# Optimization experiments

Hardware: AMD Instinct MI355X
Metric: run time of the kernel (lower is better)

The kernel has to match this reference:

```python
import jax, jax.numpy as jnp
import numpy as np

N = 50000      # nodes
E = 600000     # edges (avg degree 12)
D_IN = 16      # node_input_size
D = 128        # hidden_size
H = 4          # num_heads
DH = D // H
L = 4          # message_passing_num
D_FF = 512     # 4*hidden FFN expansion
D_OUT = 3      # output_size


def setup_inputs() -> dict:
    key = jax.random.key(0)
    ks = iter(jax.random.split(key, 32))
    def w(shape, fan_in):
        return jax.random.normal(next(ks), shape, jnp.float32) / np.float32(np.sqrt(fan_in))
    return {
        "features": jax.random.normal(next(ks), (N, D_IN), jnp.float32),
        "senders": jax.random.randint(next(ks), (E,), 0, N),
        "receivers": jax.random.randint(next(ks), (E,), 0, N),
        "enc_w1": w((D_IN, D), D_IN), "enc_b1": jnp.zeros((D,), jnp.float32),
        "enc_w2": w((D, D), D),       "enc_b2": jnp.zeros((D,), jnp.float32),
        "wq": w((L, D, D), D), "wk": w((L, D, D), D),
        "wv": w((L, D, D), D), "wo": w((L, D, D), D),
        "ln1_s": jnp.ones((L, D), jnp.float32), "ln1_b": jnp.zeros((L, D), jnp.float32),
        "ffn_w1": w((L, D, D_FF), D), "ffn_b1": jnp.zeros((L, D_FF), jnp.float32),
        "ffn_w2": w((L, D_FF, D), D_FF), "ffn_b2": jnp.zeros((L, D), jnp.float32),
        "ln2_s": jnp.ones((L, D), jnp.float32), "ln2_b": jnp.zeros((L, D), jnp.float32),
        "dec_w1": w((D, D_OUT), D), "dec_b1": jnp.zeros((D_OUT,), jnp.float32),
        "dec_w2": w((D_OUT, D_OUT), D_OUT), "dec_b2": jnp.zeros((D_OUT,), jnp.float32),
    }


def _ln(x, s, b):
    mu = x.mean(-1, keepdims=True)
    var = ((x - mu) ** 2).mean(-1, keepdims=True)
    return (x - mu) * jax.lax.rsqrt(var + 1e-5) * s + b


def _graph_mha(x, senders, receivers, wq, wk, wv, wo):
    # Adjacency-masked attention done sparsely over the edge list
    # (equivalent to softmax over the BCOO adjacency pattern).
    n = x.shape[0]
    q = (x @ wq).reshape(n, H, DH)
    k = (x @ wk).reshape(n, H, DH)
    v = (x @ wv).reshape(n, H, DH)
    scores = (q[receivers] * k[senders]).sum(-1) / np.float32(np.sqrt(DH))  # [E,H]
    m = jax.ops.segment_max(scores, receivers, num_segments=n)             # [N,H]
    m = jnp.where(jnp.isfinite(m), m, 0.0)
    a = jnp.exp(scores - m[receivers])                                      # [E,H]
    denom = jax.ops.segment_sum(a, receivers, num_segments=n)              # [N,H]
    msg = jax.ops.segment_sum(a[:, :, None] * v[senders], receivers, num_segments=n)  # [N,H,DH]
    out = (msg / (denom[:, :, None] + 1e-9)).reshape(n, D)
    return out @ wo


def reference(features, senders, receivers,
              enc_w1, enc_b1, enc_w2, enc_b2,
              wq, wk, wv, wo, ln1_s, ln1_b,
              ffn_w1, ffn_b1, ffn_w2, ffn_b2, ln2_s, ln2_b,
              dec_w1, dec_b1, dec_w2, dec_b2):
    # encode
    x = jnp.maximum(features @ enc_w1 + enc_b1, 0.0) @ enc_w2 + enc_b2     # [N,D]
    # process: L pre-LN sparse-attention transformer blocks
    for l in range(L):
        h = _ln(x, ln1_s[l], ln1_b[l])
        x = x + _graph_mha(h, senders, receivers, wq[l], wk[l], wv[l], wo[l])
        h = _ln(x, ln2_s[l], ln2_b[l])
        x = x + jnp.maximum(h @ ffn_w1[l] + ffn_b1[l], 0.0) @ ffn_w2[l] + ffn_b2[l]
    # decode
    return jnp.maximum(x @ dec_w1 + dec_b1, 0.0) @ dec_w2 + dec_b2         # [N,D_OUT]
```

## Files before the change

### kernel.cpp

```cpp
#include <hip/hip_runtime.h>
#include <hip/hip_bf16.h>
#include <math.h>

#define D     128
#define NHEAD 4
#define DH    32
#define DFF   512
#define DIN   16
#define MAXDEG 64
#define TN    16

typedef __attribute__((ext_vector_type(8))) short bf16x8;
typedef __attribute__((ext_vector_type(4))) float f32x4;
typedef __hip_bfloat16 bf16;

#define QSCALE_L2E 0.2550348838f

#define BM 128

#define WAITV(N) asm volatile("s_waitcnt vmcnt(" #N ")" ::: "memory")
#define WAITLGKM asm volatile("s_waitcnt lgkmcnt(0)" ::: "memory")
#define FENCE()  asm volatile("" ::: "memory")
#define BAR() do { FENCE(); __builtin_amdgcn_s_barrier(); FENCE(); } while (0)

__device__ __forceinline__ void gll16(const bf16* g, bf16* l) {
    __builtin_amdgcn_global_load_lds((__attribute__((address_space(1))) void*)g,
                                     (__attribute__((address_space(3))) void*)l,
                                     16, 0, 0);
}

__device__ __forceinline__ ushort bfbits(float f) {
    __hip_bfloat16 b = __float2bfloat16(f);
    return *(ushort*)&b;
}

__global__ void k_fill(const int* __restrict__ recv, const int* __restrict__ senders,
                       int* __restrict__ deg, int* __restrict__ eid, int E) {
    int e = blockIdx.x * blockDim.x + threadIdx.x;
    if (e >= E) return;
    int r = recv[e];
    int pos = atomicAdd(&deg[r], 1);
    if (pos < MAXDEG) eid[r * MAXDEG + pos] = senders[e];
}

__global__ void k_wt(const float* __restrict__ wq, const float* __restrict__ wk,
                     const float* __restrict__ wv, const float* __restrict__ wo,
                     const float* __restrict__ w1, const float* __restrict__ w2,
                     const float* __restrict__ encw2,
                     bf16* __restrict__ wqkvT, bf16* __restrict__ woT,
                     bf16* __restrict__ w1T, bf16* __restrict__ w2T,
                     bf16* __restrict__ encw2T, int* __restrict__ deg, int N) {
    int r = blockIdx.y;
    if (r == 25) {
        int i = blockIdx.x * blockDim.x + threadIdx.x;
        if (i < N) deg[i] = 0;
        return;
    }
    const float* src; bf16* dst; int K, Nout;
    if (r < 12) {
        int l = r / 3, sel = r % 3;
        src = (sel == 0 ? wq : sel == 1 ? wk : wv) + (size_t)l * D * D;
        dst = wqkvT + (size_t)l * 3 * D * D + (size_t)sel * D * D;
        K = D; Nout = D;
    } else if (r < 16) {
        int l = r - 12;
        src = wo + (size_t)l * D * D; dst = woT + (size_t)l * D * D; K = D; Nout = D;
    } else if (r < 20) {
        int l = r - 16;
        src = w1 + (size_t)l * D * DFF; dst = w1T + (size_t)l * D * DFF; K = D; Nout = DFF;
    } else if (r < 24) {
        int l = r - 20;
        src = w2 + (size_t)l * DFF * D; dst = w2T + (size_t)l * DFF * D; K = DFF; Nout = D;
    } else {
        src = encw2; dst = encw2T; K = D; Nout = D;
    }
    int total = K * Nout;
    int i = blockIdx.x * blockDim.x + threadIdx.x;
    if (i >= total) return;
    int k = i / Nout, j = i % Nout;
    dst[(size_t)j * K + k] = __float2bfloat16(src[i]);
}

__device__ __forceinline__ void load_afrag(const bf16* A, int arow, int quad,
                                           int N, bf16x8* afr) {
    const bf16* ab = A + (size_t)arow * D + quad * 8;
#pragma unroll
    for (int i = 0; i < 4; i++) {
        uint4 v = make_uint4(0u, 0u, 0u, 0u);
        if (arow < N) v = *(const uint4*)(ab + i * 32);
        afr[i] = *(bf16x8*)&v;
    }
}

__device__ __forceinline__ void stage_full(bf16* lb, const bf16* src,
                                           int wave, int lane) {
#pragma unroll
    for (int k = 0; k < 4; k++) {
        int gidx = (wave * 4 + k) * 64 + lane;
        int r = gidx >> 4, gL = gidx & 15;
        gll16(src + (size_t)r * 128 + ((gL ^ (r & 15)) * 8),
              lb + (size_t)(wave * 4 + k) * 512);
    }
}

__device__ __forceinline__ void stage_half(bf16* lb, const bf16* src, int rs,
                                           int wave, int lane) {
#pragma unroll
    for (int k = 0; k < 2; k++) {
        int gidx = (wave * 2 + k) * 64 + lane;
        int r = gidx >> 3, gL = gidx & 7;
        gll16(src + (size_t)r * rs + ((gL ^ (r & 7)) * 8),
              lb + (size_t)(wave * 2 + k) * 512);
    }
}

__device__ __forceinline__ void mfma_tile(const bf16* Wb, const bf16x8* afr,
                                          f32x4* acc, int l16, int quad) {
#pragma unroll
    for (int i = 0; i < 4; i++)
#pragma unroll
        for (int j = 0; j < 8; j++) {
            const bf16* wp = Wb + (size_t)(j * 16 + l16) * 128
                              + (size_t)((((i * 4 + quad)) ^ l16) * 8);
            acc[j] = __builtin_amdgcn_mfma_f32_16x16x32_bf16(afr[i], *(const bf16x8*)wp,
                                                             acc[j], 0, 0, 0);
        }
}

template<int OP>
__global__ __launch_bounds__(512, 2) void k_gemm(
        const bf16* __restrict__ A, const bf16* __restrict__ Bt,
        const float* __restrict__ bias,
        const float* __restrict__ lns, const float* __restrict__ lnb,
        float* x, bf16* outB, int N) {
    __shared__ alignas(16) bf16 Wsm[128 * 128];
    int m0 = blockIdx.x * BM;
    int t = threadIdx.x;
    int wave = t >> 6, lane = t & 63;
    int quad = lane >> 4, l16 = lane & 15;
    int wm = wave * 16;

    bf16x8 afr[4];
    load_afrag(A, m0 + wm + l16, quad, N, afr);
    FENCE();
    stage_full(Wsm, Bt, wave, lane);
    WAITV(0); BAR();

    int rowb = m0 + wm + quad * 4;
    float xv[8][4];
    if (OP == 2) {
#pragma unroll
        for (int j = 0; j < 8; j++)
#pragma unroll
            for (int r = 0; r < 4; r++) {
                int gr = rowb + r;
                xv[j][r] = (gr < N) ? x[(size_t)gr * D + j * 16 + l16] : 0.f;
            }
    }

    f32x4 acc[8];
#pragma unroll
    for (int j = 0; j < 8; j++) acc[j] = (f32x4){0.f, 0.f, 0.f, 0.f};
    mfma_tile(Wsm, afr, acc, l16, quad);

    float bv[8];
    if (OP == 5) {
#pragma unroll
        for (int j = 0; j < 8; j++) bv[j] = bias[j * 16 + l16];
    }
#pragma unroll
    for (int j = 0; j < 8; j++) {
#pragma unroll
        for (int r = 0; r < 4; r++) {
            int gr = rowb + r;
            if (gr >= N) continue;
            float val = acc[j][r];
            if (OP == 5) val += bv[j];
            if (OP == 2) val += xv[j][r];
            acc[j][r] = val;
        }
    }
    float lsv[8], lbv[8];
#pragma unroll
    for (int j = 0; j < 8; j++) {
        lsv[j] = lns[j * 16 + l16];
        lbv[j] = lnb[j * 16 + l16];
    }
#pragma unroll
    for (int r = 0; r < 4; r++) {
        float s1 = 0.f, s2 = 0.f;
#pragma unroll
        for (int j = 0; j < 8; j++) {
            float v = acc[j][r];
            s1 += v; s2 += v * v;
        }
        s1 += __shfl_xor(s1, 1, 64);  s2 += __shfl_xor(s2, 1, 64);
        s1 += __shfl_xor(s1, 2, 64);  s2 += __shfl_xor(s2, 2, 64);
        s1 += __shfl_xor(s1, 4, 64);  s2 += __shfl_xor(s2, 4, 64);
        s1 += __shfl_xor(s1, 8, 64);  s2 += __shfl_xor(s2, 8, 64);
        float mu = s1 * (1.f / 128.f);
        float var = s2 * (1.f / 128.f) - mu * mu;
        float rinv = rsqrtf(fmaxf(var, 0.f) + 1e-5f);
        int gr = rowb + r;
        if (gr >= N) continue;
#pragma unroll
        for (int j = 0; j < 8; j++) {
            int col = j * 16 + l16;
            float v = acc[j][r];
            x[(size_t)gr * D + col] = v;
            outB[(size_t)gr * D + col] =
                __float2bfloat16((v - mu) * rinv * lsv[j] + lbv[j]);
        }
    }
}

__global__ __launch_bounds__(512, 2) void k_qkv(
        const bf16* __restrict__ hb, const bf16* __restrict__ wqkvT,
        bf16* __restrict__ qb, bf16* __restrict__ kvb, int N) {
    __shared__ alignas(16) bf16 Wbuf[2][128 * 128];
    int m0 = blockIdx.x * BM;
    int t = threadIdx.x;
    int wave = t >> 6, lane = t & 63;
    int quad = lane >> 4, l16 = lane & 15;
    int wm = wave * 16;

    bf16x8 afr[4];
    load_afrag(hb, m0 + wm + l16, quad, N, afr);
    FENCE();
    stage_full(Wbuf[0], wqkvT + (size_t)D * D, wave, lane);
    FENCE();
    stage_full(Wbuf[1], wqkvT + (size_t)2 * D * D, wave, lane);
    FENCE();

    int rowb = m0 + wm + quad * 4;
    f32x4 ak[8], acc[8];
#pragma unroll
    for (int j = 0; j < 8; j++) ak[j] = (f32x4){0.f, 0.f, 0.f, 0.f};

    WAITV(4); BAR();
    __builtin_amdgcn_s_setprio(1);
    mfma_tile(Wbuf[0], afr, ak, l16, quad);
    __builtin_amdgcn_s_setprio(0);
    BAR();
    stage_full(Wbuf[0], wqkvT, wave, lane);
    FENCE();
#pragma unroll
    for (int j = 0; j < 8; j++) acc[j] = (f32x4){0.f, 0.f, 0.f, 0.f};
    WAITV(4); BAR();
    __builtin_amdgcn_s_setprio(1);
    mfma_tile(Wbuf[1], afr, acc, l16, quad);
    __builtin_amdgcn_s_setprio(0);

#pragma unroll
    for (int j = 0; j < 8; j++) {
        int col = j * 16 + l16;
#pragma unroll
        for (int r = 0; r < 4; r++) {
            int gr = rowb + r;
            if (gr >= N) continue;
            uint kv = (uint)bfbits(ak[j][r]) | ((uint)bfbits(acc[j][r]) << 16);
            *(uint*)&kvb[((size_t)gr * D + col) * 2] = kv;
        }
    }
    FENCE();
    if (m0 + BM <= N) { WAITV(32); } else { WAITV(0); }
    BAR();
#pragma unroll
    for (int j = 0; j < 8; j++) acc[j] = (f32x4){0.f, 0.f, 0.f, 0.f};
    __builtin_amdgcn_s_setprio(1);
    mfma_tile(Wbuf[0], afr, acc, l16, quad);
    __builtin_amdgcn_s_setprio(0);
#pragma unroll
    for (int j = 0; j < 8; j++) {
        int col = j * 16 + l16;
#pragma unroll
        for (int r = 0; r < 4; r++) {
            int gr = rowb + r;
            if (gr >= N) continue;
            qb[(size_t)gr * D + col] = __float2bfloat16(acc[j][r] * QSCALE_L2E);
        }
    }
}

__device__ __forceinline__ void stage_ffn_tile(int ts, const bf16* w1T,
                                               const bf16* w2T, bf16* Wb3,
                                               int wave, int lane) {
    int c = ts >> 2, ph = ts & 3;
    const bf16* src; int rs;
    if (ph < 2) { src = w1T + (size_t)(c * 128) * 128 + ph * 64; rs = 128; }
    else        { src = w2T + c * 128 + (ph - 2) * 64;           rs = DFF; }
    stage_half(Wb3 + (size_t)(ts % 3) * (64 * 128), src, rs, wave, lane);
}

template<int MODE>
__global__ __launch_bounds__(512, 2) void k_ffn(
        const bf16* __restrict__ hb, const bf16* __restrict__ w1T,
        const float* __restrict__ b1,
        const bf16* __restrict__ w2T, const float* __restrict__ b2,
        const float* __restrict__ lns, const float* __restrict__ lnb,
        const float* __restrict__ dw1, const float* __restrict__ db1,
        const float* __restrict__ dw2, const float* __restrict__ db2,
        float* x, bf16* outB, float* out, int N) {
    __shared__ alignas(16) bf16 Wb3[3][64 * 128];
    __shared__ alignas(16) bf16 Hsm[128 * 128];
    int m0 = blockIdx.x * BM;
    int t = threadIdx.x;
    int wave = t >> 6, lane = t & 63;
    int quad = lane >> 4, l16 = lane & 15;
    int wm = wave * 16;
    int rowb = m0 + wm + quad * 4;

    float b1pre[4][8];
#pragma unroll
    for (int c2 = 0; c2 < 4; c2++)
#pragma unroll
        for (int j = 0; j < 8; j++) b1pre[c2][j] = b1[c2 * 128 + j * 16 + l16];

    bf16x8 afr[4];
    load_afrag(hb, m0 + wm + l16, quad, N, afr);
    FENCE();
    stage_ffn_tile(0, w1T, w2T, &Wb3[0][0], wave, lane);
    FENCE();
    stage_ffn_tile(1, w1T, w2T, &Wb3[0][0], wave, lane);
    FENCE();

    f32x4 acc2[8], accP[8];
#pragma unroll
    for (int j = 0; j < 8; j++) acc2[j] = (f32x4){0.f, 0.f, 0.f, 0.f};
    float xv[8][4];

#pragma unroll
    for (int s = 0; s < 16; s++) {
        BAR();
        if (s + 2 < 16) {
            stage_ffn_tile(s + 2, w1T, w2T, &Wb3[0][0], wave, lane);
            FENCE();
        }
        if (s < 14) { WAITV(4); } else if (s == 14) { WAITV(2); } else { WAITV(0); }
        BAR();
        const bf16* Wb = &Wb3[0][0] + (size_t)(s % 3) * (64 * 128);
        int c = s >> 2, ph = s & 3;
        if (s == 15) {
#pragma unroll
            for (int j = 0; j < 8; j++)
#pragma unroll
                for (int r = 0; r < 4; r++) {
                    int gr = rowb + r;
                    xv[j][r] = (gr < N) ? x[(size_t)gr * D + j * 16 + l16] : 0.f;
                }
        }
        if (ph < 2) {
            if (ph == 0) {
#pragma unroll
                for (int j = 0; j < 8; j++) accP[j] = (f32x4){0.f, 0.f, 0.f, 0.f};
            }
            __builtin_amdgcn_s_setprio(1);
#pragma unroll
            for (int i2 = 0; i2 < 2; i2++) {
#pragma unroll
                for (int j = 0; j < 8; j++) {
                    const bf16* wp = Wb + (size_t)(j * 16 + l16) * 64
                                      + (size_t)(((i2 * 4 + quad) ^ (l16 & 7)) * 8);
                    accP[j] = __builtin_amdgcn_mfma_f32_16x16x32_bf16(
                        afr[ph * 2 + i2], *(const bf16x8*)wp, accP[j], 0, 0, 0);
                }
            }
            __builtin_amdgcn_s_setprio(0);
            if (ph == 1) {
                int rw = wm + quad * 4;
#pragma unroll
                for (int j = 0; j < 8; j++) {
                    int gb = j * 2 + (l16 >> 3), ce = l16 & 7;
#pragma unroll
                    for (int r = 0; r < 4; r++) {
                        int row = rw + r;
                        Hsm[(size_t)row * 128 + (size_t)((gb ^ (row & 15)) * 8) + ce] =
                            __float2bfloat16(fmaxf(accP[j][r] + b1pre[c][j], 0.f));
                    }
                }
                WAITLGKM;
            }
        } else {
            int h = ph - 2;
            __builtin_amdgcn_s_setprio(1);
#pragma unroll
            for (int k2 = 0; k2 < 2; k2++) {
                int ks = h * 2 + k2;
                const bf16* hp = Hsm + (size_t)(wm + l16) * 128
                                  + (size_t)(((ks * 4 + quad) ^ l16) * 8);
                bf16x8 af2 = *(const bf16x8*)hp;
#pragma unroll
                for (int j = 0; j < 8; j++) {
                    const bf16* wp = Wb + (size_t)(j * 16 + l16) * 64
                                      + (size_t)(((k2 * 4 + quad) ^ (l16 & 7)) * 8);
                    acc2[j] = __builtin_amdgcn_mfma_f32_16x16x32_bf16(
                        af2, *(const bf16x8*)wp, acc2[j], 0, 0, 0);
                }
            }
            __builtin_amdgcn_s_setprio(0);
        }
    }

    float bv[8];
#pragma unroll
    for (int j = 0; j < 8; j++) bv[j] = b2[j * 16 + l16];
#pragma unroll
    for (int j = 0; j < 8; j++) {
#pragma unroll
        for (int r = 0; r < 4; r++) {
            int gr = rowb + r;
            if (gr >= N) continue;
            acc2[j][r] += bv[j] + xv[j][r];
        }
    }
    if (MODE == 1) {
        float dw[8][3];
#pragma unroll
        for (int j = 0; j < 8; j++) {
            int col = j * 16 + l16;
#pragma unroll
            for (int cc3 = 0; cc3 < 3; cc3++) dw[j][cc3] = dw1[col * 3 + cc3];
        }
#pragma unroll
        for (int r = 0; r < 4; r++) {
            float s0 = 0.f, s1 = 0.f, s2 = 0.f;
#pragma unroll
            for (int j = 0; j < 8; j++) {
                float v = acc2[j][r];
                s0 += v * dw[j][0]; s1 += v * dw[j][1]; s2 += v * dw[j][2];
            }
            s0 += __shfl_xor(s0, 1, 64); s1 += __shfl_xor(s1, 1, 64); s2 += __shfl_xor(s2, 1, 64);
            s0 += __shfl_xor(s0, 2, 64); s1 += __shfl_xor(s1, 2, 64); s2 += __shfl_xor(s2, 2, 64);
            s0 += __shfl_xor(s0, 4, 64); s1 += __shfl_xor(s1, 4, 64); s2 += __shfl_xor(s2, 4, 64);
            s0 += __shfl_xor(s0, 8, 64); s1 += __shfl_xor(s1, 8, 64); s2 += __shfl_xor(s2, 8, 64);
            int gr = rowb + r;
            if (l16 == 0 && gr < N) {
                float t0 = fmaxf(s0 + db1[0], 0.f);
                float t1 = fmaxf(s1 + db1[1], 0.f);
                float t2 = fmaxf(s2 + db1[2], 0.f);
#pragma unroll
                for (int o = 0; o < 3; o++)
                    out[(size_t)gr * 3 + o] =
                        t0 * dw2[0 * 3 + o] + t1 * dw2[1 * 3 + o] + t2 * dw2[2 * 3 + o] + db2[o];
            }
        }
        return;
    }
    float lsv[8], lbv[8];
#pragma unroll
    for (int j = 0; j < 8; j++) {
        lsv[j] = lns[j * 16 + l16];
        lbv[j] = lnb[j * 16 + l16];
    }
#pragma unroll
    for (int r = 0; r < 4; r++) {
        float s1 = 0.f, s2 = 0.f;
#pragma unroll
        for (int j = 0; j < 8; j++) {
            float v = acc2[j][r];
            s1 += v; s2 += v * v;
        }
        s1 += __shfl_xor(s1, 1, 64);  s2 += __shfl_xor(s2, 1, 64);
        s1 += __shfl_xor(s1, 2, 64);  s2 += __shfl_xor(s2, 2, 64);
        s1 += __shfl_xor(s1, 4, 64);  s2 += __shfl_xor(s2, 4, 64);
        s1 += __shfl_xor(s1, 8, 64);  s2 += __shfl_xor(s2, 8, 64);
        float mu = s1 * (1.f / 128.f);
        float var = s2 * (1.f / 128.f) - mu * mu;
        float rinv = rsqrtf(fmaxf(var, 0.f) + 1e-5f);
        int gr = rowb + r;
        if (gr >= N) continue;
#pragma unroll
        for (int j = 0; j < 8; j++) {
            int col = j * 16 + l16;
            float v = acc2[j][r];
            x[(size_t)gr * D + col] = v;
            outB[(size_t)gr * D + col] = __float2bfloat16((v - mu) * rinv * lsv[j] + lbv[j]);
        }
    }
}

__global__ void k_enc1(const float* __restrict__ feat,
                       const float* __restrict__ w1, const float* __restrict__ b1,
                       bf16* __restrict__ hb, int N) {
    __shared__ float fsh[TN][DIN];
    int n0 = blockIdx.x * TN;
    int j = threadIdx.x;
    int nvalid = min(TN, N - n0);
    for (int idx = j; idx < TN * DIN; idx += 128) {
        int n = idx / DIN, i = idx % DIN;
        fsh[n][i] = (n < nvalid) ? feat[(n0 + n) * DIN + i] : 0.f;
    }
    __syncthreads();
    float bb = b1[j];
#pragma unroll
    for (int n = 0; n < TN; n++) {
        float a = bb;
#pragma unroll
        for (int i = 0; i < DIN; i++) a += fsh[n][i] * w1[i * D + j];
        if (n < nvalid) hb[(size_t)(n0 + n) * D + j] = __float2bfloat16(fmaxf(a, 0.f));
    }
}

__device__ __forceinline__ void attn_edge(uint4 w, bool v, float4 qv,
                                          float& l, float& a0, float& a1,
                                          float& a2, float& a3) {
    float k0 = __uint_as_float(w.x << 16), v0 = __uint_as_float(w.x & 0xFFFF0000u);
    float k1 = __uint_as_float(w.y << 16), v1 = __uint_as_float(w.y & 0xFFFF0000u);
    float k2 = __uint_as_float(w.z << 16), v2 = __uint_as_float(w.z & 0xFFFF0000u);
    float k3 = __uint_as_float(w.w << 16), v3 = __uint_as_float(w.w & 0xFFFF0000u);
    float p = qv.x * k0 + qv.y * k1 + qv.z * k2 + qv.w * k3;
    p += __shfl_xor(p, 1, 64);
    p += __shfl_xor(p, 2, 64);
    p += __shfl_xor(p, 4, 64);
    float e = v ? exp2f(p) : 0.f;
    l += e;
    a0 += e * v0; a1 += e * v1; a2 += e * v2; a3 += e * v3;
}

__global__ __launch_bounds__(256) void k_attn(
        const bf16* __restrict__ qb, const uint* __restrict__ kvb,
        const int* __restrict__ deg, const int* __restrict__ eid,
        bf16* __restrict__ out, int N) {
    int wave = threadIdx.x >> 6, lane = threadIdx.x & 63;
    int r = blockIdx.x * 4 + wave;
    if (r >= N) return;
    int g = lane & 7;
    int h = (lane >> 3) & 3;
    int slot = lane >> 5;
    int d0 = h * 32 + g * 4;
    uint2 qw = *(const uint2*)(qb + (size_t)r * D + d0);
    float4 qv;
    qv.x = __uint_as_float(qw.x << 16);
    qv.y = __uint_as_float(qw.x & 0xFFFF0000u);
    qv.z = __uint_as_float(qw.y << 16);
    qv.w = __uint_as_float(qw.y & 0xFFFF0000u);
    int cnt = min(deg[r], MAXDEG);
    const int* row = eid + (size_t)r * MAXDEG;
    const uint* kvbase = kvb + d0;
    float l = 0.f, a0 = 0.f, a1 = 0.f, a2 = 0.f, a3 = 0.f;
    for (int base = 0; base < cnt; base += 16) {
        int ss[8];
        bool vv[8];
#pragma unroll
        for (int u = 0; u < 8; u++) {
            int e = base + u * 2 + slot;
            vv[u] = e < cnt;
            ss[u] = vv[u] ? row[e] : 0;
        }
        uint4 w[8];
#pragma unroll
        for (int u = 0; u < 8; u++)
            w[u] = *(const uint4*)(kvbase + (size_t)ss[u] * D);
#pragma unroll
        for (int u = 0; u < 8; u++)
            attn_edge(w[u], vv[u], qv, l, a0, a1, a2, a3);
    }
    l  += __shfl_xor(l, 32, 64);
    a0 += __shfl_xor(a0, 32, 64);
    a1 += __shfl_xor(a1, 32, 64);
    a2 += __shfl_xor(a2, 32, 64);
    a3 += __shfl_xor(a3, 32, 64);
    if (lane < 32) {
        float inv = 1.f / (l + 1e-9f);
        bf16 o[4];
        o[0] = __float2bfloat16(a0 * inv);
        o[1] = __float2bfloat16(a1 * inv);
        o[2] = __float2bfloat16(a2 * inv);
        o[3] = __float2bfloat16(a3 * inv);
        *(uint2*)(out + (size_t)r * D + d0) = *(uint2*)o;
    }
}

extern "C" void kernel_launch(void* const* d_in, const int* in_sizes, int n_in,
                              void* d_out, int out_size, void* d_ws, size_t ws_size,
                              hipStream_t stream) {
    const float* feat    = (const float*)d_in[0];
    const int*   senders = (const int*)d_in[1];
    const int*   recv    = (const int*)d_in[2];
    const float* enc_w1  = (const float*)d_in[3];
    const float* enc_b1  = (const float*)d_in[4];
    const float* enc_w2  = (const float*)d_in[5];
    const float* enc_b2  = (const float*)d_in[6];
    const float* wq      = (const float*)d_in[7];
    const float* wk      = (const float*)d_in[8];
    const float* wv      = (const float*)d_in[9];
    const float* wo      = (const float*)d_in[10];
    const float* ln1_s   = (const float*)d_in[11];
    const float* ln1_b   = (const float*)d_in[12];
    const float* ffn_w1  = (const float*)d_in[13];
    const float* ffn_b1  = (const float*)d_in[14];
    const float* ffn_w2  = (const float*)d_in[15];
    const float* ffn_b2  = (const float*)d_in[16];
    const float* ln2_s   = (const float*)d_in[17];
    const float* ln2_b   = (const float*)d_in[18];
    const float* dec_w1  = (const float*)d_in[19];
    const float* dec_b1  = (const float*)d_in[20];
    const float* dec_w2  = (const float*)d_in[21];
    const float* dec_b2  = (const float*)d_in[22];

    int N = in_sizes[0] / DIN;
    int E = in_sizes[1];

    char* p = (char*)d_ws;
    float* x   = (float*)p;  p += (size_t)N * D * 4;
    bf16*  qb  = (bf16*)p;   p += (size_t)N * D * 2;
    bf16*  kvb = (bf16*)p;   p += (size_t)N * D * 2 * 2;
    bf16*  hb  = (bf16*)p;   p += (size_t)N * D * 2;
    int* deg   = (int*)p;    p += (size_t)N * 4;
    int* eid   = (int*)p;    p += (size_t)N * MAXDEG * 4;
    bf16* wqkvT  = (bf16*)p; p += (size_t)4 * 3 * D * D * 2;
    bf16* woT    = (bf16*)p; p += (size_t)4 * D * D * 2;
    bf16* w1T    = (bf16*)p; p += (size_t)4 * D * DFF * 2;
    bf16* w2T    = (bf16*)p; p += (size_t)4 * DFF * D * 2;
    bf16* encw2T = (bf16*)p; p += (size_t)D * D * 2;

    int gm = (N + BM - 1) / BM;

    k_wt<<<dim3(256, 26), 256, 0, stream>>>(wq, wk, wv, wo, ffn_w1, ffn_w2, enc_w2,
                                            wqkvT, woT, w1T, w2T, encw2T, deg, N);
    k_fill<<<(E + 255) / 256, 256, 0, stream>>>(recv, senders, deg, eid, E);
    k_enc1<<<(N + TN - 1) / TN, 128, 0, stream>>>(feat, enc_w1, enc_b1, hb, N);
    k_gemm<5><<<gm, 512, 0, stream>>>(hb, encw2T, enc_b2, ln1_s, ln1_b, x, hb, N);

    for (int l = 0; l < 4; l++) {
        k_qkv<<<gm, 512, 0, stream>>>(hb, wqkvT + (size_t)l * 3 * D * D, qb, kvb, N);
        k_attn<<<(N + 3) / 4, 256, 0, stream>>>(qb, (const uint*)kvb, deg, eid, hb, N);
        k_gemm<2><<<gm, 512, 0, stream>>>(hb, woT + (size_t)l * D * D,
                                          nullptr, ln2_s + l * D, ln2_b + l * D,
                                          x, hb, N);
        if (l < 3)
            k_ffn<0><<<gm, 512, 0, stream>>>(hb, w1T + (size_t)l * D * DFF,
                                             ffn_b1 + l * DFF,
                                             w2T + (size_t)l * DFF * D, ffn_b2 + l * D,
                                             ln1_s + (l + 1) * D, ln1_b + (l + 1) * D,
                                             nullptr, nullptr, nullptr, nullptr,
                                             x, hb, nullptr, N);
        else
            k_ffn<1><<<gm, 512, 0, stream>>>(hb, w1T + (size_t)l * D * DFF,
                                             ffn_b1 + l * DFF,
                                             w2T + (size_t)l * DFF * D, ffn_b2 + l * D,
                                             nullptr, nullptr,
                                             dec_w1, dec_b1, dec_w2, dec_b2,
                                             x, nullptr, (float*)d_out, N);
    }
}
```

Measured before the change: 611.6 us.

## Shrink GEMM/FFN tiles to 64 rows with 256 threads; batch attention rows with prefetch

```diff
diff --git a/kernel.cpp b/kernel.cpp
--- a/kernel.cpp
+++ b/kernel.cpp
@@ -16,7 +16,7 @@
 
 #define QSCALE_L2E 0.2550348838f
 
-#define BM 128
+#define BMQ 128
 
 #define WAITV(N) asm volatile("s_waitcnt vmcnt(" #N ")" ::: "memory")
 #define WAITLGKM asm volatile("s_waitcnt lgkmcnt(0)" ::: "memory")
@@ -49,11 +49,16 @@
                      const float* __restrict__ encw2,
                      bf16* __restrict__ wqkvT, bf16* __restrict__ woT,
                      bf16* __restrict__ w1T, bf16* __restrict__ w2T,
-                     bf16* __restrict__ encw2T, int* __restrict__ deg, int N) {
+                     bf16* __restrict__ encw2T, int* __restrict__ deg,
+                     int* __restrict__ eid, int N) {
     int r = blockIdx.y;
     if (r == 25) {
-        int i = blockIdx.x * blockDim.x + threadIdx.x;
-        if (i < N) deg[i] = 0;
+        int tot = N + N * MAXDEG;
+        for (int i = blockIdx.x * blockDim.x + threadIdx.x; i < tot;
+             i += 256 * 256) {
+            if (i < N) deg[i] = 0;
+            else eid[i - N] = 0;
+        }
         return;
     }
     const float* src; bf16* dst; int K, Nout;
@@ -92,8 +97,19 @@
     }
 }
 
-__device__ __forceinline__ void stage_full(bf16* lb, const bf16* src,
-                                           int wave, int lane) {
+__device__ __forceinline__ void stage_full256(bf16* lb, const bf16* src,
+                                              int wave, int lane) {
+#pragma unroll
+    for (int k = 0; k < 8; k++) {
+        int gidx = (wave * 8 + k) * 64 + lane;
+        int r = gidx >> 4, gL = gidx & 15;
+        gll16(src + (size_t)r * 128 + ((gL ^ (r & 15)) * 8),
+              lb + (size_t)(wave * 8 + k) * 512);
+    }
+}
+
+__device__ __forceinline__ void stage_full512(bf16* lb, const bf16* src,
+                                              int wave, int lane) {
 #pragma unroll
     for (int k = 0; k < 4; k++) {
         int gidx = (wave * 4 + k) * 64 + lane;
@@ -103,13 +119,13 @@
     }
 }
 
-__device__ __forceinline__ void stage_half(bf16* lb, const bf16* src, int rs,
-                                           int wave, int lane) {
+__device__ __forceinline__ void stage_q(bf16* lb, const bf16* src, int rs,
+                                        int wave, int lane) {
 #pragma unroll
     for (int k = 0; k < 2; k++) {
         int gidx = (wave * 2 + k) * 64 + lane;
-        int r = gidx >> 3, gL = gidx & 7;
-        gll16(src + (size_t)r * rs + ((gL ^ (r & 7)) * 8),
+        int r = gidx >> 2, gL = gidx & 3;
+        gll16(src + (size_t)r * rs + ((gL ^ ((r >> 1) & 3)) * 8),
               lb + (size_t)(wave * 2 + k) * 512);
     }
 }
@@ -128,13 +144,13 @@
 }
 
 template<int OP>
-__global__ __launch_bounds__(512, 2) void k_gemm(
+__global__ __launch_bounds__(256, 4) void k_gemm(
         const bf16* __restrict__ A, const bf16* __restrict__ Bt,
         const float* __restrict__ bias,
         const float* __restrict__ lns, const float* __restrict__ lnb,
         float* x, bf16* outB, int N) {
     __shared__ alignas(16) bf16 Wsm[128 * 128];
-    int m0 = blockIdx.x * BM;
+    int m0 = blockIdx.x * 64;
     int t = threadIdx.x;
     int wave = t >> 6, lane = t & 63;
     int quad = lane >> 4, l16 = lane & 15;
@@ -143,7 +159,7 @@
     bf16x8 afr[4];
     load_afrag(A, m0 + wm + l16, quad, N, afr);
     FENCE();
-    stage_full(Wsm, Bt, wave, lane);
+    stage_full256(Wsm, Bt, wave, lane);
     WAITV(0); BAR();
 
     int rowb = m0 + wm + quad * 4;
@@ -218,7 +234,7 @@
         const bf16* __restrict__ hb, const bf16* __restrict__ wqkvT,
         bf16* __restrict__ qb, bf16* __restrict__ kvb, int N) {
     __shared__ alignas(16) bf16 Wbuf[2][128 * 128];
-    int m0 = blockIdx.x * BM;
+    int m0 = blockIdx.x * BMQ;
     int t = threadIdx.x;
     int wave = t >> 6, lane = t & 63;
     int quad = lane >> 4, l16 = lane & 15;
@@ -227,9 +243,9 @@
     bf16x8 afr[4];
     load_afrag(hb, m0 + wm + l16, quad, N, afr);
     FENCE();
-    stage_full(Wbuf[0], wqkvT + (size_t)D * D, wave, lane);
-    FENCE();
-    stage_full(Wbuf[1], wqkvT + (size_t)2 * D * D, wave, lane);
+    stage_full512(Wbuf[0], wqkvT + (size_t)D * D, wave, lane);
+    FENCE();
+    stage_full512(Wbuf[1], wqkvT + (size_t)2 * D * D, wave, lane);
     FENCE();
 
     int rowb = m0 + wm + quad * 4;
@@ -242,7 +258,7 @@
     mfma_tile(Wbuf[0], afr, ak, l16, quad);
     __builtin_amdgcn_s_setprio(0);
     BAR();
-    stage_full(Wbuf[0], wqkvT, wave, lane);
+    stage_full512(Wbuf[0], wqkvT, wave, lane);
     FENCE();
 #pragma unroll
     for (int j = 0; j < 8; j++) acc[j] = (f32x4){0.f, 0.f, 0.f, 0.f};
@@ -263,7 +279,7 @@
         }
     }
     FENCE();
-    if (m0 + BM <= N) { WAITV(32); } else { WAITV(0); }
+    if (m0 + BMQ <= N) { WAITV(32); } else { WAITV(0); }
     BAR();
 #pragma unroll
     for (int j = 0; j < 8; j++) acc[j] = (f32x4){0.f, 0.f, 0.f, 0.f};
@@ -282,18 +298,18 @@
     }
 }
 
-__device__ __forceinline__ void stage_ffn_tile(int ts, const bf16* w1T,
-                                               const bf16* w2T, bf16* Wb3,
-                                               int wave, int lane) {
-    int c = ts >> 2, ph = ts & 3;
+__device__ __forceinline__ void stage_ffn_q(int ts, const bf16* w1T,
+                                            const bf16* w2T, bf16* Wb3,
+                                            int wave, int lane) {
+    int c = ts >> 3, p = ts & 7;
     const bf16* src; int rs;
-    if (ph < 2) { src = w1T + (size_t)(c * 128) * 128 + ph * 64; rs = 128; }
-    else        { src = w2T + c * 128 + (ph - 2) * 64;           rs = DFF; }
-    stage_half(Wb3 + (size_t)(ts % 3) * (64 * 128), src, rs, wave, lane);
+    if (p < 4) { src = w1T + (size_t)(c * 128) * 128 + p * 32;       rs = 128; }
+    else       { src = w2T + (size_t)(c * 128) + (p - 4) * 32;       rs = DFF; }
+    stage_q(Wb3 + (size_t)(ts % 3) * (32 * 128), src, rs, wave, lane);
 }
 
 template<int MODE>
-__global__ __launch_bounds__(512, 2) void k_ffn(
+__global__ __launch_bounds__(256, 4) void k_ffn(
         const bf16* __restrict__ hb, const bf16* __restrict__ w1T,
         const float* __restrict__ b1,
         const bf16* __restrict__ w2T, const float* __restrict__ b2,
@@ -301,9 +317,9 @@
         const float* __restrict__ dw1, const float* __restrict__ db1,
         const float* __restrict__ dw2, const float* __restrict__ db2,
         float* x, bf16* outB, float* out, int N) {
-    __shared__ alignas(16) bf16 Wb3[3][64 * 128];
-    __shared__ alignas(16) bf16 Hsm[128 * 128];
-    int m0 = blockIdx.x * BM;
+    __shared__ alignas(16) bf16 Wb3[3][32 * 128];
+    __shared__ alignas(16) bf16 Hsm[64 * 128];
+    int m0 = blockIdx.x * 64;
     int t = threadIdx.x;
     int wave = t >> 6, lane = t & 63;
     int quad = lane >> 4, l16 = lane & 15;
@@ -319,9 +335,9 @@
     bf16x8 afr[4];
     load_afrag(hb, m0 + wm + l16, quad, N, afr);
     FENCE();
-    stage_ffn_tile(0, w1T, w2T, &Wb3[0][0], wave, lane);
-    FENCE();
-    stage_ffn_tile(1, w1T, w2T, &Wb3[0][0], wave, lane);
+    stage_ffn_q(0, w1T, w2T, &Wb3[0][0], wave, lane);
+    FENCE();
+    stage_ffn_q(1, w1T, w2T, &Wb3[0][0], wave, lane);
     FENCE();
 
     f32x4 acc2[8], accP[8];
@@ -329,18 +345,20 @@
     for (int j = 0; j < 8; j++) acc2[j] = (f32x4){0.f, 0.f, 0.f, 0.f};
     float xv[8][4];
 
-#pragma unroll
-    for (int s = 0; s < 16; s++) {
+    int wswz = (quad ^ ((l16 >> 1) & 3)) * 8;
+
+#pragma unroll
+    for (int s = 0; s < 32; s++) {
         BAR();
-        if (s + 2 < 16) {
-            stage_ffn_tile(s + 2, w1T, w2T, &Wb3[0][0], wave, lane);
+        if (s + 2 < 32) {
+            stage_ffn_q(s + 2, w1T, w2T, &Wb3[0][0], wave, lane);
             FENCE();
         }
-        if (s < 14) { WAITV(4); } else if (s == 14) { WAITV(2); } else { WAITV(0); }
+        if (s < 30) { WAITV(4); } else if (s == 30) { WAITV(2); } else { WAITV(0); }
         BAR();
-        const bf16* Wb = &Wb3[0][0] + (size_t)(s % 3) * (64 * 128);
-        int c = s >> 2, ph = s & 3;
-        if (s == 15) {
+        const bf16* Wb = &Wb3[0][0] + (size_t)(s % 3) * (32 * 128);
+        int c = s >> 3, p = s & 7;
+        if (s == 31) {
 #pragma unroll
             for (int j = 0; j < 8; j++)
 #pragma unroll
@@ -349,24 +367,20 @@
                     xv[j][r] = (gr < N) ? x[(size_t)gr * D + j * 16 + l16] : 0.f;
                 }
         }
-        if (ph < 2) {
-            if (ph == 0) {
+        if (p < 4) {
+            if (p == 0) {
 #pragma unroll
                 for (int j = 0; j < 8; j++) accP[j] = (f32x4){0.f, 0.f, 0.f, 0.f};
             }
             __builtin_amdgcn_s_setprio(1);
 #pragma unroll
-            for (int i2 = 0; i2 < 2; i2++) {
-#pragma unroll
-                for (int j = 0; j < 8; j++) {
-                    const bf16* wp = Wb + (size_t)(j * 16 + l16) * 64
-                                      + (size_t)(((i2 * 4 + quad) ^ (l16 & 7)) * 8);
-                    accP[j] = __builtin_amdgcn_mfma_f32_16x16x32_bf16(
-                        afr[ph * 2 + i2], *(const bf16x8*)wp, accP[j], 0, 0, 0);
-                }
+            for (int j = 0; j < 8; j++) {
+                const bf16* wp = Wb + (size_t)(j * 16 + l16) * 32 + wswz;
+                accP[j] = __builtin_amdgcn_mfma_f32_16x16x32_bf16(
+                    afr[p], *(const bf16x8*)wp, accP[j], 0, 0, 0);
             }
             __builtin_amdgcn_s_setprio(0);
-            if (ph == 1) {
+            if (p == 3) {
                 int rw = wm + quad * 4;
 #pragma unroll
                 for (int j = 0; j < 8; j++) {
@@ -381,21 +395,15 @@
                 WAITLGKM;
             }
         } else {
-            int h = ph - 2;
+            int kq = p - 4;
+            bf16x8 af2 = *(const bf16x8*)(Hsm + (size_t)(wm + l16) * 128
+                              + (size_t)(((kq * 4 + quad) ^ l16) * 8));
             __builtin_amdgcn_s_setprio(1);
 #pragma unroll
-            for (int k2 = 0; k2 < 2; k2++) {
-                int ks = h * 2 + k2;
-                const bf16* hp = Hsm + (size_t)(wm + l16) * 128
-                                  + (size_t)(((ks * 4 + quad) ^ l16) * 8);
-                bf16x8 af2 = *(const bf16x8*)hp;
-#pragma unroll
-                for (int j = 0; j < 8; j++) {
-                    const bf16* wp = Wb + (size_t)(j * 16 + l16) * 64
-                                      + (size_t)(((k2 * 4 + quad) ^ (l16 & 7)) * 8);
-                    acc2[j] = __builtin_amdgcn_mfma_f32_16x16x32_bf16(
-                        af2, *(const bf16x8*)wp, acc2[j], 0, 0, 0);
-                }
+            for (int j = 0; j < 8; j++) {
+                const bf16* wp = Wb + (size_t)(j * 16 + l16) * 32 + wswz;
+                acc2[j] = __builtin_amdgcn_mfma_f32_16x16x32_bf16(
+                    af2, *(const bf16x8*)wp, acc2[j], 0, 0, 0);
             }
             __builtin_amdgcn_s_setprio(0);
         }
@@ -517,57 +525,87 @@
     a0 += e * v0; a1 += e * v1; a2 += e * v2; a3 += e * v3;
 }
 
+__device__ __forceinline__ float4 unpackq(uint2 qw) {
+    float4 qv;
+    qv.x = __uint_as_float(qw.x << 16);
+    qv.y = __uint_as_float(qw.x & 0xFFFF0000u);
+    qv.z = __uint_as_float(qw.y << 16);
+    qv.w = __uint_as_float(qw.y & 0xFFFF0000u);
+    return qv;
+}
+
 __global__ __launch_bounds__(256) void k_attn(
         const bf16* __restrict__ qb, const uint* __restrict__ kvb,
         const int* __restrict__ deg, const int* __restrict__ eid,
         bf16* __restrict__ out, int N) {
     int wave = threadIdx.x >> 6, lane = threadIdx.x & 63;
-    int r = blockIdx.x * 4 + wave;
-    if (r >= N) return;
-    int g = lane & 7;
-    int h = (lane >> 3) & 3;
-    int slot = lane >> 5;
+    int g = lane & 7, h = (lane >> 3) & 3, slot = lane >> 5;
     int d0 = h * 32 + g * 4;
-    uint2 qw = *(const uint2*)(qb + (size_t)r * D + d0);
-    float4 qv;
-    qv.x = __uint_as_float(qw.x << 16);
-    qv.y = __uint_as_float(qw.x & 0xFFFF0000u);
-    qv.z = __uint_as_float(qw.y << 16);
-    qv.w = __uint_as_float(qw.y & 0xFFFF0000u);
-    int cnt = min(deg[r], MAXDEG);
-    const int* row = eid + (size_t)r * MAXDEG;
+    int rbase = blockIdx.x * 16 + wave * 4;
+    if (rbase >= N) return;
     const uint* kvbase = kvb + d0;
-    float l = 0.f, a0 = 0.f, a1 = 0.f, a2 = 0.f, a3 = 0.f;
-    for (int base = 0; base < cnt; base += 16) {
-        int ss[8];
-        bool vv[8];
-#pragma unroll
-        for (int u = 0; u < 8; u++) {
-            int e = base + u * 2 + slot;
-            vv[u] = e < cnt;
-            ss[u] = vv[u] ? row[e] : 0;
-        }
+
+    int ssN[8];
+    {
+        const int* row = eid + (size_t)rbase * MAXDEG;
+#pragma unroll
+        for (int u = 0; u < 8; u++) ssN[u] = row[u * 2 + slot];
+    }
+    int cntN = min(deg[rbase], MAXDEG);
+    float4 qvN = unpackq(*(const uint2*)(qb + (size_t)rbase * D + d0));
+
+#pragma unroll
+    for (int i = 0; i < 4; i++) {
+        int r = rbase + i;
+        if (r >= N) return;
+        int cnt = cntN; float4 qv = qvN;
         uint4 w[8];
 #pragma unroll
         for (int u = 0; u < 8; u++)
-            w[u] = *(const uint4*)(kvbase + (size_t)ss[u] * D);
+            w[u] = *(const uint4*)(kvbase + (size_t)ssN[u] * D);
+        int rn = r + 1;
+        if (i < 3 && rn < N) {
+            const int* rowN = eid + (size_t)rn * MAXDEG;
+#pragma unroll
+            for (int u = 0; u < 8; u++) ssN[u] = rowN[u * 2 + slot];
+            cntN = min(deg[rn], MAXDEG);
+            qvN = unpackq(*(const uint2*)(qb + (size_t)rn * D + d0));
+        }
+        float l = 0.f, a0 = 0.f, a1 = 0.f, a2 = 0.f, a3 = 0.f;
 #pragma unroll
         for (int u = 0; u < 8; u++)
-            attn_edge(w[u], vv[u], qv, l, a0, a1, a2, a3);
-    }
-    l  += __shfl_xor(l, 32, 64);
-    a0 += __shfl_xor(a0, 32, 64);
-    a1 += __shfl_xor(a1, 32, 64);
-    a2 += __shfl_xor(a2, 32, 64);
-    a3 += __shfl_xor(a3, 32, 64);
-    if (lane < 32) {
-        float inv = 1.f / (l + 1e-9f);
-        bf16 o[4];
-        o[0] = __float2bfloat16(a0 * inv);
-        o[1] = __float2bfloat16(a1 * inv);
-        o[2] = __float2bfloat16(a2 * inv);
-        o[3] = __float2bfloat16(a3 * inv);
-        *(uint2*)(out + (size_t)r * D + d0) = *(uint2*)o;
+            attn_edge(w[u], (u * 2 + slot) < cnt, qv, l, a0, a1, a2, a3);
+        for (int base = 16; base < cnt; base += 16) {
+            const int* row = eid + (size_t)r * MAXDEG;
+            int ss[8]; bool vv[8];
+#pragma unroll
+            for (int u = 0; u < 8; u++) {
+                int e = base + u * 2 + slot;
+                vv[u] = e < cnt;
+                ss[u] = row[e];
+            }
+            uint4 w2_[8];
+#pragma unroll
+            for (int u = 0; u < 8; u++)
+                w2_[u] = *(const uint4*)(kvbase + (size_t)ss[u] * D);
+#pragma unroll
+            for (int u = 0; u < 8; u++)
+                attn_edge(w2_[u], vv[u], qv, l, a0, a1, a2, a3);
+        }
+        l  += __shfl_xor(l, 32, 64);
+        a0 += __shfl_xor(a0, 32, 64);
+        a1 += __shfl_xor(a1, 32, 64);
+        a2 += __shfl_xor(a2, 32, 64);
+        a3 += __shfl_xor(a3, 32, 64);
+        if (lane < 32) {
+            float inv = 1.f / (l + 1e-9f);
+            bf16 o[4];
+            o[0] = __float2bfloat16(a0 * inv);
+            o[1] = __float2bfloat16(a1 * inv);
+            o[2] = __float2bfloat16(a2 * inv);
+            o[3] = __float2bfloat16(a3 * inv);
+            *(uint2*)(out + (size_t)r * D + d0) = *(uint2*)o;
+        }
     }
 }
 
@@ -614,33 +652,34 @@
     bf16* w2T    = (bf16*)p; p += (size_t)4 * DFF * D * 2;
     bf16* encw2T = (bf16*)p; p += (size_t)D * D * 2;
 
-    int gm = (N + BM - 1) / BM;
+    int gm64 = (N + 63) / 64;
+    int gmQ  = (N + BMQ - 1) / BMQ;
 
     k_wt<<<dim3(256, 26), 256, 0, stream>>>(wq, wk, wv, wo, ffn_w1, ffn_w2, enc_w2,
-                                            wqkvT, woT, w1T, w2T, encw2T, deg, N);
+                                            wqkvT, woT, w1T, w2T, encw2T, deg, eid, N);
     k_fill<<<(E + 255) / 256, 256, 0, stream>>>(recv, senders, deg, eid, E);
     k_enc1<<<(N + TN - 1) / TN, 128, 0, stream>>>(feat, enc_w1, enc_b1, hb, N);
-    k_gemm<5><<<gm, 512, 0, stream>>>(hb, encw2T, enc_b2, ln1_s, ln1_b, x, hb, N);
+    k_gemm<5><<<gm64, 256, 0, stream>>>(hb, encw2T, enc_b2, ln1_s, ln1_b, x, hb, N);
 
     for (int l = 0; l < 4; l++) {
-        k_qkv<<<gm, 512, 0, stream>>>(hb, wqkvT + (size_t)l * 3 * D * D, qb, kvb, N);
-        k_attn<<<(N + 3) / 4, 256, 0, stream>>>(qb, (const uint*)kvb, deg, eid, hb, N);
-        k_gemm<2><<<gm, 512, 0, stream>>>(hb, woT + (size_t)l * D * D,
-                                          nullptr, ln2_s + l * D, ln2_b + l * D,
-                                          x, hb, N);
+        k_qkv<<<gmQ, 512, 0, stream>>>(hb, wqkvT + (size_t)l * 3 * D * D, qb, kvb, N);
+        k_attn<<<(N + 15) / 16, 256, 0, stream>>>(qb, (const uint*)kvb, deg, eid, hb, N);
+        k_gemm<2><<<gm64, 256, 0, stream>>>(hb, woT + (size_t)l * D * D,
+                                            nullptr, ln2_s + l * D, ln2_b + l * D,
+                                            x, hb, N);
         if (l < 3)
-            k_ffn<0><<<gm, 512, 0, stream>>>(hb, w1T + (size_t)l * D * DFF,
-                                             ffn_b1 + l * DFF,
-                                             w2T + (size_t)l * DFF * D, ffn_b2 + l * D,
-                                             ln1_s + (l + 1) * D, ln1_b + (l + 1) * D,
-                                             nullptr, nullptr, nullptr, nullptr,
-                                             x, hb, nullptr, N);
+            k_ffn<0><<<gm64, 256, 0, stream>>>(hb, w1T + (size_t)l * D * DFF,
+                                               ffn_b1 + l * DFF,
+                                               w2T + (size_t)l * DFF * D, ffn_b2 + l * D,
+                                               ln1_s + (l + 1) * D, ln1_b + (l + 1) * D,
+                                               nullptr, nullptr, nullptr, nullptr,
+                                               x, hb, nullptr, N);
         else
-            k_ffn<1><<<gm, 512, 0, stream>>>(hb, w1T + (size_t)l * D * DFF,
-                                             ffn_b1 + l * DFF,
-                                             w2T + (size_t)l * DFF * D, ffn_b2 + l * D,
-                                             nullptr, nullptr,
-                                             dec_w1, dec_b1, dec_w2, dec_b2,
-                                             x, nullptr, (float*)d_out, N);
-    }
-}
+            k_ffn<1><<<gm64, 256, 0, stream>>>(hb, w1T + (size_t)l * D * DFF,
+                                               ffn_b1 + l * DFF,
+                                               w2T + (size_t)l * DFF * D, ffn_b2 + l * D,
+                                               nullptr, nullptr,
+                                               dec_w1, dec_b1, dec_w2, dec_b2,
+                                               x, nullptr, (float*)d_out, N);
+    }
+}
```

Measured after the change: 647.2 us. 5.8% more time.
